# Optimization experiments

Hardware: AMD Instinct MI355X
Metric: run time of the kernel (lower is better)

## Reference

```python
import jax, jax.numpy as jnp
import numpy as np

B, S, D, H = 2, 2048, 1024, 16
EPS = 1e-7  # keras backend epsilon

def setup_inputs() -> dict:
    key = jax.random.key(0)
    ks = jax.random.split(key, 5)
    x = jax.random.normal(ks[0], (B, S, D), dtype=jnp.float32)
    # mem_mask convention: attend where mem_mask == 0 (causal here)
    i = jnp.arange(S)
    causal = (i[None, :] > i[:, None]).astype(jnp.float32)  # 1 = masked
    mem_mask = jnp.broadcast_to(causal[None, None], (B, 1, S, S))
    Wqkv = jax.random.normal(ks[1], (D, 3 * D), dtype=jnp.float32) * (D ** -0.5)
    W_out = jax.random.normal(ks[2], (D, D), dtype=jnp.float32) * (D ** -0.5)
    b_out = jnp.zeros((D,), dtype=jnp.float32)
    scale = jnp.ones((D,), dtype=jnp.float32)
    gate = jax.random.normal(ks[3], (D,), dtype=jnp.float32) * 0.02
    return {"x": x, "mem_mask": mem_mask, "Wqkv": Wqkv, "W_out": W_out,
            "b_out": b_out, "scale": scale, "gate": gate}

def reference(x, mem_mask, Wqkv, W_out, b_out, scale, gate):
    b, s, d = x.shape
    dh = d // H
    h = jnp.einsum('bsd,de->bse', x, Wqkv)
    q, k, v = jnp.split(h, 3, axis=-1)
    def split_heads(t):
        return t.reshape(b, s, H, dh).transpose(0, 2, 1, 3)  # [B,H,S,dh]
    q, k, v = split_heads(q), split_heads(k), split_heads(v)
    q = q * (dh ** -0.5)
    logits = jnp.einsum('bhqd,bhkd->bhqk', q, k)
    logits = logits * (mem_mask == 0.0).astype(logits.dtype)
    weights = jax.nn.relu(logits)
    o = jnp.einsum('bhqk,bhkd->bhqd', weights, v)
    o = o.transpose(0, 2, 1, 3).reshape(b, s, d)  # combine heads
    # Gated RMSNorm
    ms = jnp.mean(o * o, axis=-1, keepdims=True)
    o = scale * o * jax.lax.rsqrt(ms + EPS) * jax.nn.sigmoid(gate * o)
    return jnp.einsum('bsd,de->bse', o, W_out) + b_out
```

## Files before the change

kernel.cpp:

```cpp
#include <hip/hip_runtime.h>
#include <hip/hip_bf16.h>

typedef unsigned short u16;
typedef __attribute__((ext_vector_type(8))) short bf16x8;
typedef __attribute__((ext_vector_type(4))) short short4v;
typedef __attribute__((ext_vector_type(4))) float floatx4;
typedef __attribute__((ext_vector_type(2))) unsigned uint2v;

__device__ __forceinline__ float bf2f(u16 u) {
    unsigned v = ((unsigned)u) << 16;
    return __builtin_bit_cast(float, v);
}
__device__ __forceinline__ u16 f2bf(float f) {
    unsigned u = __builtin_bit_cast(unsigned, f);
    u += 0x7fffu + ((u >> 16) & 1u);
    return (u16)(u >> 16);
}

#define GLDS16(g, l)                                                             \
    __builtin_amdgcn_global_load_lds(                                            \
        (const __attribute__((address_space(1))) void*)(g),                      \
        (__attribute__((address_space(3))) void*)(l), 16, 0, 0)

__global__ __launch_bounds__(256) void prep(const float* __restrict__ x, u16* __restrict__ xb,
                                            float* __restrict__ oz,
                                            const float* __restrict__ Wqkv, u16* __restrict__ WqkvT,
                                            const float* __restrict__ Wout, u16* __restrict__ WoutT) {
    __shared__ u16 t[32][33];
    int blk = blockIdx.x;
    if (blk < 4096) {
        const int i = blk * 256 + threadIdx.x;
        const floatx4 v = ((const floatx4*)x)[i];
        short4v o;
#pragma unroll
        for (int j = 0; j < 4; ++j) o[j] = (short)f2bf(v[j]);
        ((short4v*)xb)[i] = o;
        const floatx4 z = {0.f, 0.f, 0.f, 0.f};
        ((floatx4*)oz)[i] = z;
        return;
    }
    const float* in; u16* out; int R, C, bx, by;
    if (blk < 4096 + 3072) { blk -= 4096; in = Wqkv; out = WqkvT; R = 1024; C = 3072; bx = blk % 96; by = blk / 96; }
    else                   { blk -= 7168; in = Wout; out = WoutT; R = 1024; C = 1024; bx = blk & 31; by = blk >> 5; }
    const int c0 = bx * 32, r0 = by * 32;
    const int xx = threadIdx.x & 31, yy = threadIdx.x >> 5;
#pragma unroll
    for (int i = 0; i < 32; i += 8) t[yy + i][xx] = f2bf(in[(size_t)(r0 + yy + i) * C + c0 + xx]);
    __syncthreads();
#pragma unroll
    for (int i = 0; i < 32; i += 8) out[(size_t)(c0 + yy + i) * R + r0 + xx] = t[xx][yy + i];
}

template <int TM, bool BIAS, typename OUT, bool VT>
__global__ __launch_bounds__(256) void gemm_bt(const u16* __restrict__ A, const u16* __restrict__ Bt,
                                               OUT* __restrict__ C, const float* __restrict__ bias,
                                               u16* __restrict__ vtp, int M, int N, int K) {
    constexpr int MI = TM / 32;
    __shared__ u16 sA[TM * 32];
    __shared__ u16 sB[128 * 32];
    const int tid = threadIdx.x;
    const int lane = tid & 63, wave = tid >> 6;
    const int l15 = lane & 15, quad = lane >> 4;
    const int row0 = blockIdx.y * TM, col0 = blockIdx.x * 128;
    const int wm = (wave & 1) * (TM / 2), wn = (wave >> 1) * 64;
    const int c_ = (tid & 3) << 3;
    floatx4 acc[MI][4] = {};
    for (int k0 = 0; k0 < K; k0 += 32) {
#pragma unroll
        for (int it = 0; it < 2; ++it) {
            const int idx = it * 256 + tid;
            const int r = idx >> 2;
            GLDS16(Bt + (size_t)(col0 + r) * K + k0 + c_, sB + idx * 8);
        }
#pragma unroll
        for (int it = 0; it < TM / 64; ++it) {
            const int idx = it * 256 + tid;
            const int r = idx >> 2;
            GLDS16(A + (size_t)(row0 + r) * K + k0 + c_, sA + idx * 8);
        }
        __syncthreads();
        bf16x8 af[MI], bfr[4];
#pragma unroll
        for (int i = 0; i < MI; ++i) af[i] = *(const bf16x8*)(sA + (wm + i * 16 + l15) * 32 + quad * 8);
#pragma unroll
        for (int j = 0; j < 4; ++j) bfr[j] = *(const bf16x8*)(sB + (wn + j * 16 + l15) * 32 + quad * 8);
#pragma unroll
        for (int i = 0; i < MI; ++i)
#pragma unroll
            for (int j = 0; j < 4; ++j)
                acc[i][j] = __builtin_amdgcn_mfma_f32_16x16x32_bf16(af[i], bfr[j], acc[i][j], 0, 0, 0);
        __syncthreads();
    }
#pragma unroll
    for (int i = 0; i < MI; ++i) {
#pragma unroll
        for (int j = 0; j < 4; ++j) {
            const int col = col0 + wn + j * 16 + l15;
            const int row = row0 + wm + i * 16 + quad * 4;
            const float b = BIAS ? bias[col] : 0.f;
            short4v pk;
#pragma unroll
            for (int r = 0; r < 4; ++r) {
                const float v = acc[i][j][r] + b;
                if constexpr (sizeof(OUT) == 2)
                    C[(size_t)(row + r) * N + col] = (OUT)f2bf(v);
                else
                    C[(size_t)(row + r) * N + col] = (OUT)v;
                if constexpr (VT) pk[r] = (short)f2bf(v * 0.125f);
            }
            if constexpr (VT) {
                if (col0 >= 2048) {
                    const int bb = row >> 11, s = row & 2047;
                    const int hd = (col - 2048) >> 6, dh = col & 63;
                    *(short4v*)(vtp + ((size_t)(bb * 16 + hd) * 64 + dh) * 2048 + s) = pk;
                }
            }
        }
    }
}

__device__ __forceinline__ void pack_store(floatx4 s, u16* dst, bool diag, int kgb, int qg) {
    float v0 = fmaxf(s[0], 0.f), v1 = fmaxf(s[1], 0.f);
    float v2 = fmaxf(s[2], 0.f), v3 = fmaxf(s[3], 0.f);
    if (diag) {
        if (kgb + 0 > qg) v0 = 0.f;
        if (kgb + 1 > qg) v1 = 0.f;
        if (kgb + 2 > qg) v2 = 0.f;
        if (kgb + 3 > qg) v3 = 0.f;
    }
    uint2v p;
    p.x = ((__builtin_bit_cast(unsigned, v0) + 0x8000u) >> 16) |
          ((__builtin_bit_cast(unsigned, v1) + 0x8000u) & 0xffff0000u);
    p.y = ((__builtin_bit_cast(unsigned, v2) + 0x8000u) >> 16) |
          ((__builtin_bit_cast(unsigned, v3) + 0x8000u) & 0xffff0000u);
    *(uint2v*)dst = p;
}

__global__ __launch_bounds__(256) void relu_attn(const u16* __restrict__ h, const u16* __restrict__ vt,
                                                 float* __restrict__ o) {
    __shared__ u16 sK[64 * 72];
    __shared__ u16 sV[64 * 72];
    __shared__ u16 sP[64 * 72];
    const int bid = blockIdx.x;
    const int bh = bid & 31;
    const int p = bid >> 5;
    int s, qt;
    if (p < 32)      { s = 0; qt = 31 - p; }
    else if (p < 56) { s = 1; qt = 31 - (p - 32); }
    else if (p < 72) { s = 2; qt = 31 - (p - 56); }
    else             { s = 3; qt = 31 - (p - 72); }
    const int b = bh >> 4, hd = bh & 15;
    const int tid = threadIdx.x, lane = tid & 63, wave = tid >> 6;
    const int l15 = lane & 15, quad = lane >> 4;
    const int q0 = qt * 64;
    const int c_lo = s * 8, c_hi = min(s * 8 + 7, qt);

    const u16* qrow = h + (size_t)(b * 2048 + q0 + wave * 16 + l15) * 3072 + hd * 64;
    bf16x8 qf0 = *(const bf16x8*)(qrow + quad * 8);
    bf16x8 qf1 = *(const bf16x8*)(qrow + 32 + quad * 8);

    floatx4 acc[4] = {};
    const u16* kbase = h + (size_t)(b * 2048) * 3072 + 1024 + hd * 64;
    const u16* vbase = vt + (size_t)bh * 64 * 2048;
    const int sr = tid >> 3;
    const int sc = (tid & 7) << 3;
    const int qg = wave * 16 + l15;

    for (int kc = c_lo; kc <= c_hi; ++kc) {
        const int c0 = kc * 64;
#pragma unroll
        for (int it = 0; it < 2; ++it) {
            const int r = it * 32 + sr;
            bf16x8 kv = *(const bf16x8*)(kbase + (size_t)(c0 + r) * 3072 + sc);
            bf16x8 vv = *(const bf16x8*)(vbase + (size_t)r * 2048 + c0 + sc);
            *(bf16x8*)(sK + r * 72 + sc) = kv;
            *(bf16x8*)(sV + r * 72 + sc) = vv;
        }
        __syncthreads();
        const bool diag = (kc == qt);
        const floatx4 z = {0.f, 0.f, 0.f, 0.f};
#pragma unroll
        for (int mt = 0; mt < 4; ++mt) {
            const bf16x8 kf0 = *(const bf16x8*)(sK + (mt * 16 + l15) * 72 + quad * 8);
            const bf16x8 kf1 = *(const bf16x8*)(sK + (mt * 16 + l15) * 72 + 32 + quad * 8);
            const int kgb = mt * 16 + quad * 4;
            floatx4 sv_ = __builtin_amdgcn_mfma_f32_16x16x32_bf16(kf0, qf0, z, 0, 0, 0);
            sv_ = __builtin_amdgcn_mfma_f32_16x16x32_bf16(kf1, qf1, sv_, 0, 0, 0);
            pack_store(sv_, sP + (size_t)qg * 72 + kgb, diag, kgb, qg);
        }
#pragma unroll
        for (int kb = 0; kb < 2; ++kb) {
            const bf16x8 pf = *(const bf16x8*)(sP + (size_t)(wave * 16 + l15) * 72 + kb * 32 + quad * 8);
#pragma unroll
            for (int nt = 0; nt < 4; ++nt) {
                const bf16x8 vf = *(const bf16x8*)(sV + (nt * 16 + l15) * 72 + kb * 32 + quad * 8);
                acc[nt] = __builtin_amdgcn_mfma_f32_16x16x32_bf16(pf, vf, acc[nt], 0, 0, 0);
            }
        }
        __syncthreads();
    }
#pragma unroll
    for (int nt = 0; nt < 4; ++nt) {
        const int col = hd * 64 + nt * 16 + l15;
        const int row = q0 + wave * 16 + quad * 4;
#pragma unroll
        for (int r = 0; r < 4; ++r)
            atomicAdd(&o[(size_t)(b * 2048 + row + r) * 1024 + col], acc[nt][r]);
    }
}

__global__ __launch_bounds__(256) void rms_gate(const float* __restrict__ o, const float* __restrict__ scale,
                                                const float* __restrict__ gate, u16* __restrict__ out) {
    const int row = blockIdx.x;
    const int tid = threadIdx.x;
    const floatx4* op = (const floatx4*)(o + (size_t)row * 1024);
    floatx4 v = op[tid];
    float ss = v[0] * v[0] + v[1] * v[1] + v[2] * v[2] + v[3] * v[3];
#pragma unroll
    for (int m = 32; m >= 1; m >>= 1) ss += __shfl_xor(ss, m, 64);
    __shared__ float red[4];
    if ((tid & 63) == 0) red[tid >> 6] = ss;
    __syncthreads();
    const float ms = (red[0] + red[1] + red[2] + red[3]) * (1.0f / 1024.0f);
    const float inv = rsqrtf(ms + 1e-7f);
    const int c = tid * 4;
#pragma unroll
    for (int j = 0; j < 4; ++j) {
        const float s = scale[c + j];
        const float g = gate[c + j];
        const float x = v[j];
        const float sig = 1.0f / (1.0f + __expf(-g * x));
        out[(size_t)row * 1024 + c + j] = f2bf(s * x * inv * sig);
    }
}

extern "C" void kernel_launch(void* const* d_in, const int* in_sizes, int n_in,
                              void* d_out, int out_size, void* d_ws, size_t ws_size,
                              hipStream_t stream) {
    const float* x     = (const float*)d_in[0];
    const float* Wqkv  = (const float*)d_in[2];
    const float* Wout  = (const float*)d_in[3];
    const float* bout  = (const float*)d_in[4];
    const float* scale = (const float*)d_in[5];
    const float* gate  = (const float*)d_in[6];
    float* out = (float*)d_out;

    char* p = (char*)d_ws;
    u16* xb    = (u16*)p; p += (size_t)4096 * 1024 * 2;
    u16* h     = (u16*)p; p += (size_t)4096 * 3072 * 2;
    u16* vt    = (u16*)p; p += (size_t)32 * 64 * 2048 * 2;
    u16* WqkvT = (u16*)p; p += (size_t)3072 * 1024 * 2;
    u16* WoutT = (u16*)p; p += (size_t)1024 * 1024 * 2;
    float* oat = (float*)p; p += (size_t)4096 * 1024 * 4;
    u16* onorm = (u16*)p; p += (size_t)4096 * 1024 * 2;

    prep<<<8192, 256, 0, stream>>>(x, xb, oat, Wqkv, WqkvT, Wout, WoutT);
    gemm_bt<128, false, u16, true><<<dim3(24, 32), 256, 0, stream>>>(xb, WqkvT, h, nullptr, vt, 4096, 3072, 1024);
    relu_attn<<<2560, 256, 0, stream>>>(h, vt, oat);
    rms_gate<<<4096, 256, 0, stream>>>(oat, scale, gate, onorm);
    gemm_bt<64, true, float, false><<<dim3(8, 64), 256, 0, stream>>>(onorm, WoutT, out, bout, nullptr, 4096, 1024, 1024);
}
```

Measured before the change: 223.6 us.

## Share K/V tiles across four query tiles per block in relu attention

Restructures the attention kernel so each block covers 256 queries, one 64-query tile per wave, against a 256-key split, instead of 64 queries split across 4 waves. Each K/V tile staged in shared memory is now reused by four query tiles, which cuts global loads and block count (1152 vs 2560). In exchange it uses more registers (16 accumulators plus 8 Q fragments per lane) and per-wave P buffers. Waves whose query tile lies before the key chunk sit idle, so the causal triangle is unbalanced within a block.

```diff
diff --git a/kernel.cpp b/kernel.cpp
--- a/kernel.cpp
+++ b/kernel.cpp
@@ -140,33 +140,43 @@
                                                  float* __restrict__ o) {
     __shared__ u16 sK[64 * 72];
     __shared__ u16 sV[64 * 72];
-    __shared__ u16 sP[64 * 72];
+    __shared__ u16 sPall[4][64 * 34];
     const int bid = blockIdx.x;
     const int bh = bid & 31;
-    const int p = bid >> 5;
-    int s, qt;
-    if (p < 32)      { s = 0; qt = 31 - p; }
-    else if (p < 56) { s = 1; qt = 31 - (p - 32); }
-    else if (p < 72) { s = 2; qt = 31 - (p - 56); }
-    else             { s = 3; qt = 31 - (p - 72); }
+    const int j = bid >> 5;
+    int s, gq;
+    if      (j < 8)  { s = 0; gq = j; }
+    else if (j < 15) { s = 1; gq = j - 7; }
+    else if (j < 21) { s = 2; gq = j - 13; }
+    else if (j < 26) { s = 3; gq = j - 18; }
+    else if (j < 30) { s = 4; gq = j - 22; }
+    else if (j < 33) { s = 5; gq = j - 25; }
+    else if (j < 35) { s = 6; gq = j - 27; }
+    else             { s = 7; gq = 7; }
     const int b = bh >> 4, hd = bh & 15;
     const int tid = threadIdx.x, lane = tid & 63, wave = tid >> 6;
     const int l15 = lane & 15, quad = lane >> 4;
+    u16* sP = sPall[wave];
+    const int qt = 4 * gq + wave;
     const int q0 = qt * 64;
-    const int c_lo = s * 8, c_hi = min(s * 8 + 7, qt);
-
-    const u16* qrow = h + (size_t)(b * 2048 + q0 + wave * 16 + l15) * 3072 + hd * 64;
-    bf16x8 qf0 = *(const bf16x8*)(qrow + quad * 8);
-    bf16x8 qf1 = *(const bf16x8*)(qrow + 32 + quad * 8);
-
-    floatx4 acc[4] = {};
+
+    bf16x8 qf[4][2];
+    {
+        const u16* qb = h + (size_t)(b * 2048 + q0) * 3072 + hd * 64;
+#pragma unroll
+        for (int qc = 0; qc < 4; ++qc)
+#pragma unroll
+            for (int ks = 0; ks < 2; ++ks)
+                qf[qc][ks] = *(const bf16x8*)(qb + (size_t)(qc * 16 + l15) * 3072 + ks * 32 + quad * 8);
+    }
+
+    floatx4 acc[4][4] = {};
     const u16* kbase = h + (size_t)(b * 2048) * 3072 + 1024 + hd * 64;
     const u16* vbase = vt + (size_t)bh * 64 * 2048;
     const int sr = tid >> 3;
     const int sc = (tid & 7) << 3;
-    const int qg = wave * 16 + l15;
-
-    for (int kc = c_lo; kc <= c_hi; ++kc) {
+
+    for (int kc = 4 * s; kc <= 4 * s + 3; ++kc) {
         const int c0 = kc * 64;
 #pragma unroll
         for (int it = 0; it < 2; ++it) {
@@ -177,35 +187,49 @@
             *(bf16x8*)(sV + r * 72 + sc) = vv;
         }
         __syncthreads();
-        const bool diag = (kc == qt);
-        const floatx4 z = {0.f, 0.f, 0.f, 0.f};
-#pragma unroll
-        for (int mt = 0; mt < 4; ++mt) {
-            const bf16x8 kf0 = *(const bf16x8*)(sK + (mt * 16 + l15) * 72 + quad * 8);
-            const bf16x8 kf1 = *(const bf16x8*)(sK + (mt * 16 + l15) * 72 + 32 + quad * 8);
-            const int kgb = mt * 16 + quad * 4;
-            floatx4 sv_ = __builtin_amdgcn_mfma_f32_16x16x32_bf16(kf0, qf0, z, 0, 0, 0);
-            sv_ = __builtin_amdgcn_mfma_f32_16x16x32_bf16(kf1, qf1, sv_, 0, 0, 0);
-            pack_store(sv_, sP + (size_t)qg * 72 + kgb, diag, kgb, qg);
-        }
-#pragma unroll
-        for (int kb = 0; kb < 2; ++kb) {
-            const bf16x8 pf = *(const bf16x8*)(sP + (size_t)(wave * 16 + l15) * 72 + kb * 32 + quad * 8);
-#pragma unroll
-            for (int nt = 0; nt < 4; ++nt) {
-                const bf16x8 vf = *(const bf16x8*)(sV + (nt * 16 + l15) * 72 + kb * 32 + quad * 8);
-                acc[nt] = __builtin_amdgcn_mfma_f32_16x16x32_bf16(pf, vf, acc[nt], 0, 0, 0);
+        if (kc <= qt) {
+            const bool diag = (kc == qt);
+            const floatx4 z = {0.f, 0.f, 0.f, 0.f};
+#pragma unroll
+            for (int kb = 0; kb < 2; ++kb) {
+#pragma unroll
+                for (int mt = 0; mt < 2; ++mt) {
+                    const bf16x8 kf0 = *(const bf16x8*)(sK + (kb * 32 + mt * 16 + l15) * 72 + quad * 8);
+                    const bf16x8 kf1 = *(const bf16x8*)(sK + (kb * 32 + mt * 16 + l15) * 72 + 32 + quad * 8);
+#pragma unroll
+                    for (int qc = 0; qc < 4; ++qc) {
+                        floatx4 sv_ = __builtin_amdgcn_mfma_f32_16x16x32_bf16(kf0, qf[qc][0], z, 0, 0, 0);
+                        sv_ = __builtin_amdgcn_mfma_f32_16x16x32_bf16(kf1, qf[qc][1], sv_, 0, 0, 0);
+                        pack_store(sv_, sP + (qc * 16 + l15) * 34 + mt * 16 + quad * 4,
+                                   diag, kb * 32 + mt * 16 + quad * 4, qc * 16 + l15);
+                    }
+                }
+                bf16x8 vf[4], pf[4];
+#pragma unroll
+                for (int nt = 0; nt < 4; ++nt)
+                    vf[nt] = *(const bf16x8*)(sV + (nt * 16 + l15) * 72 + kb * 32 + quad * 8);
+#pragma unroll
+                for (int qr = 0; qr < 4; ++qr)
+                    pf[qr] = *(const bf16x8*)(sP + (qr * 16 + l15) * 34 + quad * 8);
+#pragma unroll
+                for (int qr = 0; qr < 4; ++qr)
+#pragma unroll
+                    for (int nt = 0; nt < 4; ++nt)
+                        acc[qr][nt] = __builtin_amdgcn_mfma_f32_16x16x32_bf16(pf[qr], vf[nt], acc[qr][nt], 0, 0, 0);
             }
         }
         __syncthreads();
     }
 #pragma unroll
-    for (int nt = 0; nt < 4; ++nt) {
-        const int col = hd * 64 + nt * 16 + l15;
-        const int row = q0 + wave * 16 + quad * 4;
-#pragma unroll
-        for (int r = 0; r < 4; ++r)
-            atomicAdd(&o[(size_t)(b * 2048 + row + r) * 1024 + col], acc[nt][r]);
+    for (int qr = 0; qr < 4; ++qr) {
+#pragma unroll
+        for (int nt = 0; nt < 4; ++nt) {
+            const int col = hd * 64 + nt * 16 + l15;
+            const int row = b * 2048 + q0 + qr * 16 + quad * 4;
+#pragma unroll
+            for (int r = 0; r < 4; ++r)
+                atomicAdd(&o[(size_t)(row + r) * 1024 + col], acc[qr][nt][r]);
+        }
     }
 }
 
@@ -256,7 +280,7 @@
 
     prep<<<8192, 256, 0, stream>>>(x, xb, oat, Wqkv, WqkvT, Wout, WoutT);
     gemm_bt<128, false, u16, true><<<dim3(24, 32), 256, 0, stream>>>(xb, WqkvT, h, nullptr, vt, 4096, 3072, 1024);
-    relu_attn<<<2560, 256, 0, stream>>>(h, vt, oat);
+    relu_attn<<<1152, 256, 0, stream>>>(h, vt, oat);
     rms_gate<<<4096, 256, 0, stream>>>(oat, scale, gate, onorm);
     gemm_bt<64, true, float, false><<<dim3(8, 64), 256, 0, stream>>>(onorm, WoutT, out, bout, nullptr, 4096, 1024, 1024);
 }
```

Result: slower. 261.8 us (+17.1%).
